# Performance work log

Measured on AMD Instinct MI355X. Metric: run time of the kernel, lower is better.

The kernel has to match this reference:

```python
import jax, jax.numpy as jnp
import numpy as np

B, T, C, H, L, V = 512, 128, 512, 8, 6, 13
D = C // H  # 64


def setup_inputs() -> dict:
    key = jax.random.key(0)
    ks = jax.random.split(key, 12)
    s = 0.02
    return {
        "token_idxs": jax.random.randint(ks[0], (B, T), 0, V),
        "label": jax.random.randint(ks[1], (B,), 0, V),
        "wte": jax.random.normal(ks[2], (V, C), jnp.float32) * s,
        "wpe": jax.random.normal(ks[3], (T, C), jnp.float32) * s,
        "Wq": jax.random.normal(ks[4], (L, C, C), jnp.float32) * s,
        "bq": jnp.zeros((L, C), jnp.float32),
        "Wk": jax.random.normal(ks[5], (L, C, C), jnp.float32) * s,
        "bk": jnp.zeros((L, C), jnp.float32),
        "Wv": jax.random.normal(ks[6], (L, C, C), jnp.float32) * s,
        "bv": jnp.zeros((L, C), jnp.float32),
        "Wo": jax.random.normal(ks[7], (L, C, C), jnp.float32) * s,
        "bo": jnp.zeros((L, C), jnp.float32),
        "ln_g": jnp.ones((L, C), jnp.float32),
        "ln_b": jnp.zeros((L, C), jnp.float32),
        "W_lm": jax.random.normal(ks[8], (C, V), jnp.float32) * s,
        "b_lm": jnp.zeros((V,), jnp.float32),
    }


def _layer_norm(x, g, b, eps=1e-5):
    m = jnp.mean(x, axis=-1, keepdims=True)
    v = jnp.var(x, axis=-1, keepdims=True)
    return (x - m) / jnp.sqrt(v + eps) * g + b


def reference(token_idxs, label, wte, wpe, Wq, bq, Wk, bk, Wv, bv, Wo, bo, ln_g, ln_b, W_lm, b_lm):
    b, t = token_idxs.shape
    x = wte[token_idxs] + wpe[jnp.arange(t)]  # [b,t,C]
    inv_sqrt_d = 1.0 / jnp.sqrt(jnp.float32(D))
    for i in range(L):
        q = (x @ Wq[i] + bq[i]).reshape(b, t, H, D)
        k = (x @ Wk[i] + bk[i]).reshape(b, t, H, D)
        v = (x @ Wv[i] + bv[i]).reshape(b, t, H, D)
        # NOTE: matches the source exactly: attention over the HEAD axis at
        # each (b,t) position -> att shape [b,t,H,H]
        att = jnp.einsum('bthd,btgd->bthg', q, k) * inv_sqrt_d
        att = jax.nn.softmax(att, axis=-1)
        hid = jnp.einsum('bthg,btgd->bthd', att, v).reshape(b, t, C)
        x = _layer_norm(hid @ Wo[i] + bo[i] + x, ln_g[i], ln_b[i])
    logits = x @ W_lm + b_lm  # [b,t,V]
    logp = jax.nn.log_softmax(logits[:, -1, :], axis=-1)
    loss = -jnp.take_along_axis(logp, label[:, None], axis=-1).mean()
    return logits, loss
```

## Files before the change

kernel.cpp:

```cpp
#include <hip/hip_runtime.h>
#include <hip/hip_bf16.h>
#include <cstdint>
#include <cstddef>


typedef __attribute__((ext_vector_type(8))) short short8;
typedef __attribute__((ext_vector_type(4))) float f32x4;

__device__ __forceinline__ float bf2f(ushort u) {
    return __uint_as_float(((unsigned int)u) << 16);
}
__device__ __forceinline__ ushort f2bf(float f) {
    unsigned int x = __float_as_uint(f);
    unsigned int r = (x + 0x7fffu + ((x >> 16) & 1u)) >> 16;
    return (ushort)r;
}
__device__ __forceinline__ void gload_lds16(const void* g, void* l) {
    __builtin_amdgcn_global_load_lds(
        (const __attribute__((address_space(1))) void*)g,
        (__attribute__((address_space(3))) void*)l, 16, 0, 0);
}

__global__ __launch_bounds__(256) void prep_all(
    const float* __restrict__ Wq, const float* __restrict__ Wk,
    const float* __restrict__ Wv, const float* __restrict__ Wo,
    const float* __restrict__ wte, const float* __restrict__ wpe,
    ushort* __restrict__ wqkvT, ushort* __restrict__ woT,
    ushort* __restrict__ x0) {
    __shared__ float lds[64][65];
    const int bid = blockIdx.x;
    const int tid = threadIdx.x;
    if (bid < 1536) {
        const int mat = bid >> 6;
        const int tile = bid & 63;
        const int tr = tile >> 3, tc = tile & 7;
        const int l = mat >> 2, which = mat & 3;
        const float* S;
        switch (which) {
            case 0: S = Wq; break;
            case 1: S = Wk; break;
            case 2: S = Wv; break;
            default: S = Wo; break;
        }
        S += (size_t)l * 262144;
        ushort* T = (which < 3) ? wqkvT + (size_t)l * 786432 + which * 262144
                                : woT + (size_t)l * 262144;
        const int c = tid & 63;
        #pragma unroll
        for (int it = 0; it < 16; it++) {
            int r = it * 4 + (tid >> 6);
            lds[r][c] = S[(size_t)(tr * 64 + r) * 512 + tc * 64 + c];
        }
        __syncthreads();
        #pragma unroll
        for (int it = 0; it < 16; it++) {
            int r = it * 4 + (tid >> 6);
            T[(size_t)(tc * 64 + r) * 512 + tr * 64 + c] = f2bf(lds[c][r]);
        }
    } else {
        size_t idx = (size_t)(bid - 1536) * 256 + tid;
        size_t u = idx >> 6;
        int c8 = (int)(idx & 63);
        int v = (int)(u >> 7);
        int t = (int)(u & 127);
        const float* ep = wte + (size_t)v * 512 + c8 * 8;
        const float* pp = wpe + (size_t)t * 512 + c8 * 8;
        float4 e0 = *(const float4*)ep, e1 = *(const float4*)(ep + 4);
        float4 p0 = *(const float4*)pp, p1 = *(const float4*)(pp + 4);
        float s[8] = {e0.x + p0.x, e0.y + p0.y, e0.z + p0.z, e0.w + p0.w,
                      e1.x + p1.x, e1.y + p1.y, e1.z + p1.z, e1.w + p1.w};
        short8 o;
        #pragma unroll
        for (int j = 0; j < 8; j++) o[j] = (short)f2bf(s[j]);
        *(short8*)(x0 + u * 512 + c8 * 8) = o;
    }
}

__global__ __launch_bounds__(256) void gemm_qkv_kernel(
    const ushort* __restrict__ A, const ushort* __restrict__ Bt,
    const float* __restrict__ b0, const float* __restrict__ b1,
    const float* __restrict__ b2, ushort* __restrict__ obf) {
    __shared__ alignas(16) ushort As[2][64 * 64];
    __shared__ alignas(16) ushort Bs[2][128 * 64];
    const int tid = threadIdx.x;
    const int lane = tid & 63;
    const int wave = tid >> 6;
    const int m0 = blockIdx.x * 64;
    const int n0 = blockIdx.y * 128;
    const int wm = (wave >> 1) * 32;
    const int wn = (wave & 1) * 64;
    const int r = lane & 15;
    const int kq = (lane >> 4) * 8;
    const ushort* Ab = A  + (size_t)m0 * 512;
    const ushort* Bb = Bt + (size_t)n0 * 512;
    f32x4 acc[2][4] = {};

    auto stage = [&](int t, int b) {
        const ushort* At = Ab + t * 64;
        const ushort* Bt2 = Bb + t * 64;
        #pragma unroll
        for (int i = 0; i < 2; i++) {
            int cb = (i * 4 + wave) * 64;
            int ch = cb + lane;
            int row = ch >> 3;
            int c8 = (ch & 7) ^ (row & 7);
            gload_lds16(At + (size_t)row * 512 + c8 * 8, (char*)As[b] + cb * 16);
        }
        #pragma unroll
        for (int i = 0; i < 4; i++) {
            int cb = (i * 4 + wave) * 64;
            int ch = cb + lane;
            int row = ch >> 3;
            int c8 = (ch & 7) ^ (row & 7);
            gload_lds16(Bt2 + (size_t)row * 512 + c8 * 8, (char*)Bs[b] + cb * 16);
        }
    };

    stage(0, 0);
    __syncthreads();
    #pragma unroll
    for (int t = 0; t < 8; t++) {
        const int cur = t & 1;
        if (t < 7) stage(t + 1, cur ^ 1);
        #pragma unroll
        for (int kk = 0; kk < 64; kk += 32) {
            short8 af[2], bfr[4];
            #pragma unroll
            for (int m = 0; m < 2; m++) {
                int row = wm + m * 16 + r;
                int boff = (row * 128 + (kk + kq) * 2) ^ ((row & 7) << 4);
                af[m] = *(const short8*)((const char*)As[cur] + boff);
            }
            #pragma unroll
            for (int n = 0; n < 4; n++) {
                int row = wn + n * 16 + r;
                int boff = (row * 128 + (kk + kq) * 2) ^ ((row & 7) << 4);
                bfr[n] = *(const short8*)((const char*)Bs[cur] + boff);
            }
            #pragma unroll
            for (int m = 0; m < 2; m++)
                #pragma unroll
                for (int n = 0; n < 4; n++)
                    acc[m][n] = __builtin_amdgcn_mfma_f32_16x16x32_bf16(
                        af[m], bfr[n], acc[m][n], 0, 0, 0);
        }
        __syncthreads();
    }
    const int r4 = (lane >> 4) * 4;
    const int cc = lane & 15;
    #pragma unroll
    for (int m = 0; m < 2; m++) {
        #pragma unroll
        for (int n = 0; n < 4; n++) {
            int cg = n0 + wn + n * 16 + cc;
            float bias = (cg < 512) ? b0[cg] : (cg < 1024) ? b1[cg - 512] : b2[cg - 1024];
            #pragma unroll
            for (int i = 0; i < 4; i++) {
                int rg = m0 + wm + m * 16 + r4 + i;
                obf[(size_t)rg * 1536 + cg] = f2bf(acc[m][n][i] + bias);
            }
        }
    }
}

__global__ __launch_bounds__(256) void attn_proj(
    const ushort* __restrict__ qkv, const ushort* __restrict__ Bt,
    const float* __restrict__ bo_, const ushort* __restrict__ xres,
    ushort* __restrict__ tmp, float* __restrict__ ps, float* __restrict__ pss) {
    __shared__ alignas(16) ushort Hs[8][32 * 64];
    __shared__ alignas(16) ushort Bs[2][128 * 64];
    __shared__ float lps[2][32], lpss[2][32];
    const int tid = threadIdx.x;
    const int lane = tid & 63;
    const int wave = tid >> 6;
    const int m0 = blockIdx.x * 32;
    const int n0 = blockIdx.y * 128;

    const ushort* Bb = Bt + (size_t)n0 * 512;
    auto stageB = [&](int t, int b) {
        const ushort* Bt2 = Bb + t * 64;
        #pragma unroll
        for (int i = 0; i < 4; i++) {
            int cb = (i * 4 + wave) * 64;
            int ch = cb + lane;
            int row = ch >> 3;
            int c8 = (ch & 7) ^ (row & 7);
            gload_lds16(Bt2 + (size_t)row * 512 + c8 * 8, (char*)Bs[b] + cb * 16);
        }
    };
    stageB(0, 0);

    {
        const int h = lane >> 3, g = lane & 7;
        #pragma unroll
        for (int it = 0; it < 8; it++) {
            int lrow = wave * 8 + it;
            const ushort* base = qkv + (size_t)(m0 + lrow) * 1536;
            const ushort* qp = base + h * 64;
            const ushort* kp = base + 512 + g * 64;
            float s = 0.f;
            #pragma unroll
            for (int dc = 0; dc < 8; dc++) {
                short8 q8 = *(const short8*)(qp + dc * 8);
                short8 k8 = *(const short8*)(kp + dc * 8);
                #pragma unroll
                for (int j = 0; j < 8; j++) s += bf2f((ushort)q8[j]) * bf2f((ushort)k8[j]);
            }
            s *= 0.125f;
            float mx = s;
            #pragma unroll
            for (int o = 1; o < 8; o <<= 1) mx = fmaxf(mx, __shfl_xor(mx, o));
            float e = __expf(s - mx);
            float den = e;
            #pragma unroll
            for (int o = 1; o < 8; o <<= 1) den += __shfl_xor(den, o);
            float att = e / den;
            float o8[8];
            #pragma unroll
            for (int j = 0; j < 8; j++) o8[j] = 0.f;
            const ushort* vp = base + 1024 + (lane & 7) * 8;
            #pragma unroll
            for (int gg = 0; gg < 8; gg++) {
                float a = __shfl(att, (lane & 56) | gg);
                short8 v8 = *(const short8*)(vp + gg * 64);
                #pragma unroll
                for (int j = 0; j < 8; j++) o8[j] += a * bf2f((ushort)v8[j]);
            }
            short8 ov;
            #pragma unroll
            for (int j = 0; j < 8; j++) ov[j] = (short)f2bf(o8[j]);
            int off = (lrow * 128 + (lane & 7) * 16) ^ ((lrow & 7) << 4);
            *(short8*)((char*)Hs[lane >> 3] + off) = ov;
        }
    }
    __syncthreads();

    const int r = lane & 15;
    const int kq = (lane >> 4) * 8;
    const int wm = (wave >> 1) * 16;
    const int wn = (wave & 1) * 64;
    f32x4 acc[4] = {};
    #pragma unroll
    for (int t = 0; t < 8; t++) {
        const int cur = t & 1;
        if (t < 7) stageB(t + 1, cur ^ 1);
        #pragma unroll
        for (int kk = 0; kk < 64; kk += 32) {
            int arow = wm + r;
            int aoff = (arow * 128 + (kk + kq) * 2) ^ ((arow & 7) << 4);
            short8 af = *(const short8*)((const char*)Hs[t] + aoff);
            #pragma unroll
            for (int n = 0; n < 4; n++) {
                int brow = wn + n * 16 + r;
                int boff = (brow * 128 + (kk + kq) * 2) ^ ((brow & 7) << 4);
                short8 bfr = *(const short8*)((const char*)Bs[cur] + boff);
                acc[n] = __builtin_amdgcn_mfma_f32_16x16x32_bf16(
                    af, bfr, acc[n], 0, 0, 0);
            }
        }
        __syncthreads();
    }

    const int r4 = (lane >> 4) * 4;
    const int cc = lane & 15;
    float s_i[4] = {0.f, 0.f, 0.f, 0.f}, ss_i[4] = {0.f, 0.f, 0.f, 0.f};
    #pragma unroll
    for (int n = 0; n < 4; n++) {
        int col = n0 + wn + n * 16 + cc;
        float bias = bo_[col];
        #pragma unroll
        for (int i = 0; i < 4; i++) {
            int rg = m0 + wm + r4 + i;
            float v = acc[n][i] + bias + bf2f(xres[(size_t)rg * 512 + col]);
            tmp[(size_t)rg * 512 + col] = f2bf(v);
            s_i[i] += v; ss_i[i] += v * v;
        }
    }
    #pragma unroll
    for (int i = 0; i < 4; i++) {
        #pragma unroll
        for (int o = 1; o < 16; o <<= 1) {
            s_i[i] += __shfl_xor(s_i[i], o);
            ss_i[i] += __shfl_xor(ss_i[i], o);
        }
    }
    if (cc == 0) {
        #pragma unroll
        for (int i = 0; i < 4; i++) {
            lps[wave & 1][wm + r4 + i] = s_i[i];
            lpss[wave & 1][wm + r4 + i] = ss_i[i];
        }
    }
    __syncthreads();
    if (tid < 32) {
        int row = m0 + tid;
        ps[blockIdx.y * 1664 + row]  = lps[0][tid] + lps[1][tid];
        pss[blockIdx.y * 1664 + row] = lpss[0][tid] + lpss[1][tid];
    }
}

__global__ __launch_bounds__(256) void ln_finalize_kernel(
    const ushort* __restrict__ tmp, const float* __restrict__ ps,
    const float* __restrict__ pss, const float* __restrict__ gw,
    const float* __restrict__ bw, ushort* __restrict__ xbf) {
    const int lane = threadIdx.x & 63;
    const size_t row = (size_t)blockIdx.x * 4 + (threadIdx.x >> 6);
    float s  = ps[row]  + ps[1664 + row]  + ps[2 * 1664 + row]  + ps[3 * 1664 + row];
    float ss = pss[row] + pss[1664 + row] + pss[2 * 1664 + row] + pss[3 * 1664 + row];
    float mean = s * (1.f / 512.f);
    float var = ss * (1.f / 512.f) - mean * mean;
    float rstd = rsqrtf(var + 1e-5f);
    short8 tv = *(const short8*)(tmp + row * 512 + lane * 8);
    const float* gp = gw + lane * 8;
    const float* bp = bw + lane * 8;
    float4 g0 = *(const float4*)gp, g1 = *(const float4*)(gp + 4);
    float4 b0 = *(const float4*)bp, b1 = *(const float4*)(bp + 4);
    float gg[8] = {g0.x, g0.y, g0.z, g0.w, g1.x, g1.y, g1.z, g1.w};
    float bb[8] = {b0.x, b0.y, b0.z, b0.w, b1.x, b1.y, b1.z, b1.w};
    short8 o;
    #pragma unroll
    for (int j = 0; j < 8; j++)
        o[j] = (short)f2bf((bf2f((ushort)tv[j]) - mean) * rstd * gg[j] + bb[j]);
    *(short8*)(xbf + row * 512 + lane * 8) = o;
}

__global__ __launch_bounds__(256) void logits_ln(
    const ushort* __restrict__ tin, const float* __restrict__ psin,
    const float* __restrict__ pssin, const float* __restrict__ gv,
    const float* __restrict__ bv, const float* __restrict__ Wlm,
    const float* __restrict__ blm, float* __restrict__ lu) {
    __shared__ float wl[8 * 64 * 13];
    const int tid = threadIdx.x;
    for (int k = tid; k < 512; k += 256) {
        int dst = ((k & 7) * 64 + (k >> 3)) * 13;
        #pragma unroll
        for (int v = 0; v < 13; v++) wl[dst + v] = Wlm[k * 13 + v];
    }
    __syncthreads();
    const int lane = tid & 63;
    const int w = tid >> 6;
    const int c0 = lane * 8;
    float4 g0 = *(const float4*)(gv + c0), g1 = *(const float4*)(gv + c0 + 4);
    float4 b0 = *(const float4*)(bv + c0), b1 = *(const float4*)(bv + c0 + 4);
    float gg[8] = {g0.x, g0.y, g0.z, g0.w, g1.x, g1.y, g1.z, g1.w};
    float bb[8] = {b0.x, b0.y, b0.z, b0.w, b1.x, b1.y, b1.z, b1.w};
    float bl[13];
    #pragma unroll
    for (int v = 0; v < 13; v++) bl[v] = blm[v];
    for (int it = 0; it < 8; it++) {
        size_t row = (size_t)blockIdx.x * 32 + it * 4 + w;
        float s  = psin[row] + psin[1664 + row] + psin[3328 + row] + psin[4992 + row];
        float ss = pssin[row] + pssin[1664 + row] + pssin[3328 + row] + pssin[4992 + row];
        float mean = s * (1.f / 512.f);
        float rstd = rsqrtf(ss * (1.f / 512.f) - mean * mean + 1e-5f);
        short8 xv = *(const short8*)(tin + row * 512 + c0);
        float p[13];
        #pragma unroll
        for (int v = 0; v < 13; v++) p[v] = 0.f;
        #pragma unroll
        for (int j = 0; j < 8; j++) {
            float xf = (bf2f((ushort)xv[j]) - mean) * rstd * gg[j] + bb[j];
            const float* wr = wl + (j * 64 + lane) * 13;
            #pragma unroll
            for (int v = 0; v < 13; v++) p[v] += xf * wr[v];
        }
        #pragma unroll
        for (int v = 0; v < 13; v++) {
            #pragma unroll
            for (int o = 32; o > 0; o >>= 1) p[v] += __shfl_xor(p[v], o);
        }
        if (lane == 0) {
            #pragma unroll
            for (int v = 0; v < 13; v++) lu[row * 13 + v] = p[v] + bl[v];
        }
    }
}

__global__ __launch_bounds__(256) void scatter_loss(
    const float* __restrict__ lu, const int* __restrict__ tok,
    const int* __restrict__ label, float* __restrict__ out) {
    __shared__ float red[4];
    const int tid = threadIdx.x;
    if (blockIdx.x < 3328) {
        unsigned int i = blockIdx.x * 256 + tid;
        unsigned int bt = i / 13u;
        unsigned int vv = i - bt * 13u;
        int v = tok[bt];
        int t = (int)(bt & 127u);
        out[i] = lu[(size_t)((v << 7) + t) * 13 + vv];
    } else {
        float acc = 0.f;
        for (int b = tid; b < 512; b += 256) {
            int v = tok[b * 128 + 127];
            const float* lg = lu + (size_t)((v << 7) + 127) * 13;
            float mx = lg[0];
            #pragma unroll
            for (int vv = 1; vv < 13; vv++) mx = fmaxf(mx, lg[vv]);
            float den = 0.f;
            #pragma unroll
            for (int vv = 0; vv < 13; vv++) den += expf(lg[vv] - mx);
            int lab = label[b];
            acc += -(lg[lab] - mx - logf(den));
        }
        #pragma unroll
        for (int o = 32; o > 0; o >>= 1) acc += __shfl_xor(acc, o);
        if ((tid & 63) == 0) red[tid >> 6] = acc;
        __syncthreads();
        if (tid == 0)
            out[851968] = (red[0] + red[1] + red[2] + red[3]) * (1.f / 512.f);
    }
}

extern "C" void kernel_launch(void* const* d_in, const int* in_sizes, int n_in,
                              void* d_out, int out_size, void* d_ws, size_t ws_size,
                              hipStream_t stream) {
    const int*   tok   = (const int*)d_in[0];
    const int*   label = (const int*)d_in[1];
    const float* wte   = (const float*)d_in[2];
    const float* wpe   = (const float*)d_in[3];
    const float* Wq    = (const float*)d_in[4];
    const float* bq    = (const float*)d_in[5];
    const float* Wk    = (const float*)d_in[6];
    const float* bk    = (const float*)d_in[7];
    const float* Wv    = (const float*)d_in[8];
    const float* bv    = (const float*)d_in[9];
    const float* Wo    = (const float*)d_in[10];
    const float* bo    = (const float*)d_in[11];
    const float* ln_g  = (const float*)d_in[12];
    const float* ln_b  = (const float*)d_in[13];
    const float* Wlm   = (const float*)d_in[14];
    const float* blm   = (const float*)d_in[15];
    float* out = (float*)d_out;

    char* ws = (char*)d_ws;
    ushort* xbf   = (ushort*)(ws);
    ushort* wqkvT = (ushort*)(ws + 1703936);
    ushort* woT   = (ushort*)(ws + 11141120);
    ushort* qkv_u = (ushort*)(ws + 14286848);
    ushort* tmp   = (ushort*)(ws + 19398656);
    float*  lu    = (float*) (ws + 21102592);
    float*  ps    = (float*) (ws + 21189120);
    float*  pss   = (float*) (ws + 21215744);

    prep_all<<<1952, 256, 0, stream>>>(Wq, Wk, Wv, Wo, wte, wpe, wqkvT, woT, xbf);

    for (int l = 0; l < 6; l++) {
        gemm_qkv_kernel<<<dim3(26, 12), 256, 0, stream>>>(
            xbf, wqkvT + (size_t)l * 786432,
            bq + l * 512, bk + l * 512, bv + l * 512, qkv_u);
        attn_proj<<<dim3(52, 4), 256, 0, stream>>>(
            qkv_u, woT + (size_t)l * 262144, bo + l * 512, xbf, tmp, ps, pss);
        if (l < 5)
            ln_finalize_kernel<<<416, 256, 0, stream>>>(
                tmp, ps, pss, ln_g + l * 512, ln_b + l * 512, xbf);
    }

    logits_ln<<<52, 256, 0, stream>>>(tmp, ps, pss,
                                      ln_g + 5 * 512, ln_b + 5 * 512, Wlm, blm, lu);
    scatter_loss<<<3329, 256, 0, stream>>>(lu, tok, label, out);
}
```

Before: 254.3 us.

## Fold LayerNorm into QKV weights and epilogues, split attention into its own kernel

Removes the separate ln_finalize kernel. The previous layer's gamma is folded into the QKV weights during prep, and per-column sums of gamma*W and beta*W are precomputed so the QKV GEMM epilogue can apply mean and rstd per row. The output projection now normalizes the residual on the fly, and attention moves out of the projection kernel into a standalone kernel that writes a hid buffer. This saves one full activation read/write pass per layer, but adds an extra kernel launch and an extra round trip of hid through global memory, plus possible precision drift from the algebraic fold.

```diff
diff --git a/kernel.cpp b/kernel.cpp
--- a/kernel.cpp
+++ b/kernel.cpp
@@ -25,15 +25,20 @@
     const float* __restrict__ Wq, const float* __restrict__ Wk,
     const float* __restrict__ Wv, const float* __restrict__ Wo,
     const float* __restrict__ wte, const float* __restrict__ wpe,
+    const float* __restrict__ ln_g, const float* __restrict__ ln_b,
     ushort* __restrict__ wqkvT, ushort* __restrict__ woT,
-    ushort* __restrict__ x0) {
+    ushort* __restrict__ tmp0, float* __restrict__ s_qkv,
+    float* __restrict__ t_qkv, float* __restrict__ psA,
+    float* __restrict__ pssA, float* __restrict__ ones,
+    float* __restrict__ zeros) {
     __shared__ float lds[64][65];
+    __shared__ float gld[64], bld[64];
+    __shared__ float sred[4][64], tred[4][64];
     const int bid = blockIdx.x;
     const int tid = threadIdx.x;
-    if (bid < 1536) {
-        const int mat = bid >> 6;
-        const int tile = bid & 63;
-        const int tr = tile >> 3, tc = tile & 7;
+    if (bid < 192) {
+        const int mat = bid >> 3;
+        const int tc = bid & 7;
         const int l = mat >> 2, which = mat & 3;
         const float* S;
         switch (which) {
@@ -45,20 +50,55 @@
         S += (size_t)l * 262144;
         ushort* T = (which < 3) ? wqkvT + (size_t)l * 786432 + which * 262144
                                 : woT + (size_t)l * 262144;
+        const bool fold = (which < 3);
+        const float* g = (fold && l > 0) ? ln_g + (l - 1) * 512 : nullptr;
+        const float* b = (fold && l > 0) ? ln_b + (l - 1) * 512 : nullptr;
         const int c = tid & 63;
-        #pragma unroll
-        for (int it = 0; it < 16; it++) {
-            int r = it * 4 + (tid >> 6);
-            lds[r][c] = S[(size_t)(tr * 64 + r) * 512 + tc * 64 + c];
-        }
-        __syncthreads();
-        #pragma unroll
-        for (int it = 0; it < 16; it++) {
-            int r = it * 4 + (tid >> 6);
-            T[(size_t)(tc * 64 + r) * 512 + tr * 64 + c] = f2bf(lds[c][r]);
-        }
-    } else {
-        size_t idx = (size_t)(bid - 1536) * 256 + tid;
+        float sp = 0.f, tp = 0.f;
+        for (int tr = 0; tr < 8; tr++) {
+            __syncthreads();
+            #pragma unroll
+            for (int it = 0; it < 16; it++) {
+                int r = it * 4 + (tid >> 6);
+                lds[r][c] = S[(size_t)(tr * 64 + r) * 512 + tc * 64 + c];
+            }
+            if (tid < 64) {
+                gld[tid] = g ? g[tr * 64 + tid] : 1.f;
+                bld[tid] = b ? b[tr * 64 + tid] : 0.f;
+            }
+            __syncthreads();
+            float gk = fold ? gld[c] : 1.f;
+            #pragma unroll
+            for (int it = 0; it < 16; it++) {
+                int rn = it * 4 + (tid >> 6);
+                float val = lds[c][rn] * gk;
+                T[(size_t)(tc * 64 + rn) * 512 + tr * 64 + c] = f2bf(val);
+            }
+            if (fold) {
+                #pragma unroll
+                for (int i = 0; i < 16; i++) {
+                    int kl = (tid >> 6) * 16 + i;
+                    float w = lds[kl][c];
+                    sp += gld[kl] * w;
+                    tp += bld[kl] * w;
+                }
+            }
+        }
+        if (fold) {
+            __syncthreads();
+            sred[tid >> 6][c] = sp;
+            tred[tid >> 6][c] = tp;
+            __syncthreads();
+            if (tid < 64) {
+                float ss = sred[0][tid] + sred[1][tid] + sred[2][tid] + sred[3][tid];
+                float tt = tred[0][tid] + tred[1][tid] + tred[2][tid] + tred[3][tid];
+                int o = l * 1536 + which * 512 + tc * 64 + tid;
+                s_qkv[o] = ss;
+                t_qkv[o] = tt;
+            }
+        }
+    } else if (bid < 608) {
+        size_t idx = (size_t)(bid - 192) * 256 + tid;
         size_t u = idx >> 6;
         int c8 = (int)(idx & 63);
         int v = (int)(u >> 7);
@@ -72,16 +112,29 @@
         short8 o;
         #pragma unroll
         for (int j = 0; j < 8; j++) o[j] = (short)f2bf(s[j]);
-        *(short8*)(x0 + u * 512 + c8 * 8) = o;
-    }
-}
-
-__global__ __launch_bounds__(256) void gemm_qkv_kernel(
-    const ushort* __restrict__ A, const ushort* __restrict__ Bt,
+        *(short8*)(tmp0 + u * 512 + c8 * 8) = o;
+    } else if (bid < 660) {
+        int i = (bid - 608) * 256 + tid;
+        if (i < 6656) psA[i] = 0.f;
+        else {
+            int j = i - 6656;
+            pssA[j] = (j < 1664) ? 511.99488f : 0.f;
+        }
+    } else {
+        ones[tid] = 1.f;  ones[tid + 256] = 1.f;
+        zeros[tid] = 0.f; zeros[tid + 256] = 0.f;
+    }
+}
+
+__global__ __launch_bounds__(256) void qkv_fold(
+    const ushort* __restrict__ A, const float* __restrict__ psin,
+    const float* __restrict__ pssin, const ushort* __restrict__ Bt,
+    const float* __restrict__ s_l, const float* __restrict__ t_l,
     const float* __restrict__ b0, const float* __restrict__ b1,
     const float* __restrict__ b2, ushort* __restrict__ obf) {
     __shared__ alignas(16) ushort As[2][64 * 64];
     __shared__ alignas(16) ushort Bs[2][128 * 64];
+    __shared__ float smu[64], srs[64];
     const int tid = threadIdx.x;
     const int lane = tid & 63;
     const int wave = tid >> 6;
@@ -117,6 +170,15 @@
     };
 
     stage(0, 0);
+    if (tid < 64) {
+        int row = m0 + tid;
+        float s  = psin[row] + psin[1664 + row] + psin[3328 + row] + psin[4992 + row];
+        float ss = pssin[row] + pssin[1664 + row] + pssin[3328 + row] + pssin[4992 + row];
+        float mean = s * (1.f / 512.f);
+        float var = ss * (1.f / 512.f) - mean * mean;
+        smu[tid] = mean;
+        srs[tid] = rsqrtf(var + 1e-5f);
+    }
     __syncthreads();
     #pragma unroll
     for (int t = 0; t < 8; t++) {
@@ -154,31 +216,93 @@
         for (int n = 0; n < 4; n++) {
             int cg = n0 + wn + n * 16 + cc;
             float bias = (cg < 512) ? b0[cg] : (cg < 1024) ? b1[cg - 512] : b2[cg - 1024];
+            float sc = s_l[cg];
+            float tc_ = t_l[cg] + bias;
             #pragma unroll
             for (int i = 0; i < 4; i++) {
-                int rg = m0 + wm + m * 16 + r4 + i;
-                obf[(size_t)rg * 1536 + cg] = f2bf(acc[m][n][i] + bias);
-            }
-        }
-    }
-}
-
-__global__ __launch_bounds__(256) void attn_proj(
-    const ushort* __restrict__ qkv, const ushort* __restrict__ Bt,
-    const float* __restrict__ bo_, const ushort* __restrict__ xres,
-    ushort* __restrict__ tmp, float* __restrict__ ps, float* __restrict__ pss) {
-    __shared__ alignas(16) ushort Hs[8][32 * 64];
+                int lrow = wm + m * 16 + r4 + i;
+                float v = srs[lrow] * (acc[m][n][i] - smu[lrow] * sc) + tc_;
+                obf[(size_t)(m0 + lrow) * 1536 + cg] = f2bf(v);
+            }
+        }
+    }
+}
+
+__global__ __launch_bounds__(256) void attn_kernel(const ushort* __restrict__ qkv,
+                                                   ushort* __restrict__ hid) {
+    const int lane = threadIdx.x & 63;
+    const size_t pos = (size_t)blockIdx.x * 4 + (threadIdx.x >> 6);
+    const ushort* base = qkv + pos * 1536;
+    const int h = lane >> 3, g = lane & 7;
+    const ushort* qp = base + h * 64;
+    const ushort* kp = base + 512 + g * 64;
+    float s = 0.f;
+    #pragma unroll
+    for (int dc = 0; dc < 8; dc++) {
+        short8 q8 = *(const short8*)(qp + dc * 8);
+        short8 k8 = *(const short8*)(kp + dc * 8);
+        #pragma unroll
+        for (int j = 0; j < 8; j++) s += bf2f((ushort)q8[j]) * bf2f((ushort)k8[j]);
+    }
+    s *= 0.125f;
+    float mx = s;
+    #pragma unroll
+    for (int o = 1; o < 8; o <<= 1) mx = fmaxf(mx, __shfl_xor(mx, o));
+    float e = __expf(s - mx);
+    float den = e;
+    #pragma unroll
+    for (int o = 1; o < 8; o <<= 1) den += __shfl_xor(den, o);
+    float att = e / den;
+    float o8[8];
+    #pragma unroll
+    for (int j = 0; j < 8; j++) o8[j] = 0.f;
+    const ushort* vp = base + 1024 + (lane & 7) * 8;
+    #pragma unroll
+    for (int gg = 0; gg < 8; gg++) {
+        float a = __shfl(att, (lane & 56) | gg);
+        short8 v8 = *(const short8*)(vp + gg * 64);
+        #pragma unroll
+        for (int j = 0; j < 8; j++) o8[j] += a * bf2f((ushort)v8[j]);
+    }
+    short8 ov;
+    #pragma unroll
+    for (int j = 0; j < 8; j++) ov[j] = (short)f2bf(o8[j]);
+    *(short8*)(hid + pos * 512 + lane * 8) = ov;
+}
+
+__global__ __launch_bounds__(256) void proj_fold(
+    const ushort* __restrict__ A, const ushort* __restrict__ Bt,
+    const float* __restrict__ bo_, const float* __restrict__ psin,
+    const float* __restrict__ pssin, const float* __restrict__ g_in,
+    const float* __restrict__ b_in, ushort* tmp,
+    float* __restrict__ psout, float* __restrict__ pssout) {
+    __shared__ alignas(16) ushort As[2][32 * 64];
     __shared__ alignas(16) ushort Bs[2][128 * 64];
     __shared__ float lps[2][32], lpss[2][32];
+    __shared__ float smu[32], srs[32];
     const int tid = threadIdx.x;
     const int lane = tid & 63;
     const int wave = tid >> 6;
     const int m0 = blockIdx.x * 32;
     const int n0 = blockIdx.y * 128;
-
+    const int wm = (wave >> 1) * 16;
+    const int wn = (wave & 1) * 64;
+    const int r = lane & 15;
+    const int kq = (lane >> 4) * 8;
+    const ushort* Ab = A  + (size_t)m0 * 512;
     const ushort* Bb = Bt + (size_t)n0 * 512;
-    auto stageB = [&](int t, int b) {
+    f32x4 acc[4] = {};
+
+    auto stage = [&](int t, int b) {
+        const ushort* At = Ab + t * 64;
         const ushort* Bt2 = Bb + t * 64;
+        {
+            int cb = wave * 64;
+            int ch = cb + lane;
+            int row = ch >> 3;
+            int c8 = (ch & 7) ^ (row & 7);
+            gload_lds16(At + (size_t)row * 512 + c8 * 8, (char*)As[b] + cb * 16);
+        }
         #pragma unroll
         for (int i = 0; i < 4; i++) {
             int cb = (i * 4 + wave) * 64;
@@ -188,67 +312,27 @@
             gload_lds16(Bt2 + (size_t)row * 512 + c8 * 8, (char*)Bs[b] + cb * 16);
         }
     };
-    stageB(0, 0);
-
-    {
-        const int h = lane >> 3, g = lane & 7;
-        #pragma unroll
-        for (int it = 0; it < 8; it++) {
-            int lrow = wave * 8 + it;
-            const ushort* base = qkv + (size_t)(m0 + lrow) * 1536;
-            const ushort* qp = base + h * 64;
-            const ushort* kp = base + 512 + g * 64;
-            float s = 0.f;
-            #pragma unroll
-            for (int dc = 0; dc < 8; dc++) {
-                short8 q8 = *(const short8*)(qp + dc * 8);
-                short8 k8 = *(const short8*)(kp + dc * 8);
-                #pragma unroll
-                for (int j = 0; j < 8; j++) s += bf2f((ushort)q8[j]) * bf2f((ushort)k8[j]);
-            }
-            s *= 0.125f;
-            float mx = s;
-            #pragma unroll
-            for (int o = 1; o < 8; o <<= 1) mx = fmaxf(mx, __shfl_xor(mx, o));
-            float e = __expf(s - mx);
-            float den = e;
-            #pragma unroll
-            for (int o = 1; o < 8; o <<= 1) den += __shfl_xor(den, o);
-            float att = e / den;
-            float o8[8];
-            #pragma unroll
-            for (int j = 0; j < 8; j++) o8[j] = 0.f;
-            const ushort* vp = base + 1024 + (lane & 7) * 8;
-            #pragma unroll
-            for (int gg = 0; gg < 8; gg++) {
-                float a = __shfl(att, (lane & 56) | gg);
-                short8 v8 = *(const short8*)(vp + gg * 64);
-                #pragma unroll
-                for (int j = 0; j < 8; j++) o8[j] += a * bf2f((ushort)v8[j]);
-            }
-            short8 ov;
-            #pragma unroll
-            for (int j = 0; j < 8; j++) ov[j] = (short)f2bf(o8[j]);
-            int off = (lrow * 128 + (lane & 7) * 16) ^ ((lrow & 7) << 4);
-            *(short8*)((char*)Hs[lane >> 3] + off) = ov;
-        }
+
+    stage(0, 0);
+    if (tid < 32) {
+        int row = m0 + tid;
+        float s  = psin[row] + psin[1664 + row] + psin[3328 + row] + psin[4992 + row];
+        float ss = pssin[row] + pssin[1664 + row] + pssin[3328 + row] + pssin[4992 + row];
+        float mean = s * (1.f / 512.f);
+        float var = ss * (1.f / 512.f) - mean * mean;
+        smu[tid] = mean;
+        srs[tid] = rsqrtf(var + 1e-5f);
     }
     __syncthreads();
-
-    const int r = lane & 15;
-    const int kq = (lane >> 4) * 8;
-    const int wm = (wave >> 1) * 16;
-    const int wn = (wave & 1) * 64;
-    f32x4 acc[4] = {};
     #pragma unroll
     for (int t = 0; t < 8; t++) {
         const int cur = t & 1;
-        if (t < 7) stageB(t + 1, cur ^ 1);
+        if (t < 7) stage(t + 1, cur ^ 1);
         #pragma unroll
         for (int kk = 0; kk < 64; kk += 32) {
             int arow = wm + r;
             int aoff = (arow * 128 + (kk + kq) * 2) ^ ((arow & 7) << 4);
-            short8 af = *(const short8*)((const char*)Hs[t] + aoff);
+            short8 af = *(const short8*)((const char*)As[cur] + aoff);
             #pragma unroll
             for (int n = 0; n < 4; n++) {
                 int brow = wn + n * 16 + r;
@@ -267,11 +351,15 @@
     #pragma unroll
     for (int n = 0; n < 4; n++) {
         int col = n0 + wn + n * 16 + cc;
-        float bias = bo_[col];
+        float boc = bo_[col];
+        float gc = g_in[col], bc = b_in[col];
         #pragma unroll
         for (int i = 0; i < 4; i++) {
-            int rg = m0 + wm + r4 + i;
-            float v = acc[n][i] + bias + bf2f(xres[(size_t)rg * 512 + col]);
+            int lr = wm + r4 + i;
+            int rg = m0 + lr;
+            float resid = (bf2f(tmp[(size_t)rg * 512 + col]) - smu[lr])
+                          * srs[lr] * gc + bc;
+            float v = acc[n][i] + boc + resid;
             tmp[(size_t)rg * 512 + col] = f2bf(v);
             s_i[i] += v; ss_i[i] += v * v;
         }
@@ -287,41 +375,16 @@
     if (cc == 0) {
         #pragma unroll
         for (int i = 0; i < 4; i++) {
-            lps[wave & 1][wm + r4 + i] = s_i[i];
-            lpss[wave & 1][wm + r4 + i] = ss_i[i];
+            lps[wn >> 6][wm + r4 + i] = s_i[i];
+            lpss[wn >> 6][wm + r4 + i] = ss_i[i];
         }
     }
     __syncthreads();
     if (tid < 32) {
         int row = m0 + tid;
-        ps[blockIdx.y * 1664 + row]  = lps[0][tid] + lps[1][tid];
-        pss[blockIdx.y * 1664 + row] = lpss[0][tid] + lpss[1][tid];
-    }
-}
-
-__global__ __launch_bounds__(256) void ln_finalize_kernel(
-    const ushort* __restrict__ tmp, const float* __restrict__ ps,
-    const float* __restrict__ pss, const float* __restrict__ gw,
-    const float* __restrict__ bw, ushort* __restrict__ xbf) {
-    const int lane = threadIdx.x & 63;
-    const size_t row = (size_t)blockIdx.x * 4 + (threadIdx.x >> 6);
-    float s  = ps[row]  + ps[1664 + row]  + ps[2 * 1664 + row]  + ps[3 * 1664 + row];
-    float ss = pss[row] + pss[1664 + row] + pss[2 * 1664 + row] + pss[3 * 1664 + row];
-    float mean = s * (1.f / 512.f);
-    float var = ss * (1.f / 512.f) - mean * mean;
-    float rstd = rsqrtf(var + 1e-5f);
-    short8 tv = *(const short8*)(tmp + row * 512 + lane * 8);
-    const float* gp = gw + lane * 8;
-    const float* bp = bw + lane * 8;
-    float4 g0 = *(const float4*)gp, g1 = *(const float4*)(gp + 4);
-    float4 b0 = *(const float4*)bp, b1 = *(const float4*)(bp + 4);
-    float gg[8] = {g0.x, g0.y, g0.z, g0.w, g1.x, g1.y, g1.z, g1.w};
-    float bb[8] = {b0.x, b0.y, b0.z, b0.w, b1.x, b1.y, b1.z, b1.w};
-    short8 o;
-    #pragma unroll
-    for (int j = 0; j < 8; j++)
-        o[j] = (short)f2bf((bf2f((ushort)tv[j]) - mean) * rstd * gg[j] + bb[j]);
-    *(short8*)(xbf + row * 512 + lane * 8) = o;
+        psout[blockIdx.y * 1664 + row]  = lps[0][tid] + lps[1][tid];
+        pssout[blockIdx.y * 1664 + row] = lpss[0][tid] + lpss[1][tid];
+    }
 }
 
 __global__ __launch_bounds__(256) void logits_ln(
@@ -433,29 +496,43 @@
     float* out = (float*)d_out;
 
     char* ws = (char*)d_ws;
-    ushort* xbf   = (ushort*)(ws);
-    ushort* wqkvT = (ushort*)(ws + 1703936);
-    ushort* woT   = (ushort*)(ws + 11141120);
-    ushort* qkv_u = (ushort*)(ws + 14286848);
+    ushort* wqkvT = (ushort*)(ws);
+    ushort* woT   = (ushort*)(ws + 9437184);
+    ushort* qkv_u = (ushort*)(ws + 12582912);
+    ushort* hid_u = (ushort*)(ws + 17694720);
     ushort* tmp   = (ushort*)(ws + 19398656);
-    float*  lu    = (float*) (ws + 21102592);
-    float*  ps    = (float*) (ws + 21189120);
-    float*  pss   = (float*) (ws + 21215744);
-
-    prep_all<<<1952, 256, 0, stream>>>(Wq, Wk, Wv, Wo, wte, wpe, wqkvT, woT, xbf);
-
+    float*  psA   = (float*) (ws + 21102592);
+    float*  pssA  = (float*) (ws + 21129216);
+    float*  psB   = (float*) (ws + 21155840);
+    float*  pssB  = (float*) (ws + 21182464);
+    float*  lu    = (float*) (ws + 21209088);
+    float*  s_qkv = (float*) (ws + 21295616);
+    float*  t_qkv = (float*) (ws + 21332480);
+    float*  ones  = (float*) (ws + 21369344);
+    float*  zeros = (float*) (ws + 21371392);
+
+    prep_all<<<661, 256, 0, stream>>>(Wq, Wk, Wv, Wo, wte, wpe, ln_g, ln_b,
+                                      wqkvT, woT, tmp, s_qkv, t_qkv,
+                                      psA, pssA, ones, zeros);
+
+    const float *psin = psA, *pssin = pssA;
+    float *psout = psB, *pssout = pssB;
     for (int l = 0; l < 6; l++) {
-        gemm_qkv_kernel<<<dim3(26, 12), 256, 0, stream>>>(
-            xbf, wqkvT + (size_t)l * 786432,
+        const float* g_in = (l == 0) ? ones  : ln_g + (l - 1) * 512;
+        const float* b_in = (l == 0) ? zeros : ln_b + (l - 1) * 512;
+        qkv_fold<<<dim3(26, 12), 256, 0, stream>>>(
+            tmp, psin, pssin, wqkvT + (size_t)l * 786432,
+            s_qkv + l * 1536, t_qkv + l * 1536,
             bq + l * 512, bk + l * 512, bv + l * 512, qkv_u);
-        attn_proj<<<dim3(52, 4), 256, 0, stream>>>(
-            qkv_u, woT + (size_t)l * 262144, bo + l * 512, xbf, tmp, ps, pss);
-        if (l < 5)
-            ln_finalize_kernel<<<416, 256, 0, stream>>>(
-                tmp, ps, pss, ln_g + l * 512, ln_b + l * 512, xbf);
-    }
-
-    logits_ln<<<52, 256, 0, stream>>>(tmp, ps, pss,
+        attn_kernel<<<416, 256, 0, stream>>>(qkv_u, hid_u);
+        proj_fold<<<dim3(52, 4), 256, 0, stream>>>(
+            hid_u, woT + (size_t)l * 262144, bo + l * 512,
+            psin, pssin, g_in, b_in, tmp, psout, pssout);
+        const float* p1 = psin;  psin = psout;  psout = (float*)p1;
+        const float* p2 = pssin; pssin = pssout; pssout = (float*)p2;
+    }
+
+    logits_ln<<<52, 256, 0, stream>>>(tmp, psin, pssin,
                                       ln_g + 5 * 512, ln_b + 5 * 512, Wlm, blm, lu);
     scatter_loss<<<3329, 256, 0, stream>>>(lu, tok, label, out);
 }
```

New measurement: 220.4 us. -13.3%, faster.
